# Performance work log

Measured on AMD Instinct MI355X. Metric: run time of the kernel, lower is better.

## Reference

```python
import jax, jax.numpy as jnp
import numpy as np
from math import factorial, sqrt

L_MAX = 3
L_MAX_OUT = 3
NUM_SHELLS = 3
NUM_SH = (L_MAX + 1) ** 2  # 16 spherical-harmonic kernel components
SPLIT = [2 * l + 1 for l in range(L_MAX + 1)]  # [1,3,5,7]


def _su2_cg(j1, m1, j2, m2, j3, m3):
    """Clebsch-Gordan coefficient <j1 m1 j2 m2 | j3 m3> via the Racah formula."""
    if m3 != m1 + m2:
        return 0.0
    f = factorial
    vmin = max(-j1 + j2 + m3, -j1 + m1, 0)
    vmax = min(j2 + j3 + m1, j3 - j1 + j2, j3 + m3)
    c = sqrt((2 * j3 + 1) * f(j3 + j1 - j2) * f(j3 - j1 + j2) * f(j1 + j2 - j3) / f(j1 + j2 + j3 + 1)
             * f(j3 + m3) * f(j3 - m3) / (f(j1 - m1) * f(j1 + m1) * f(j2 - m2) * f(j2 + m2)))
    s = 0.0
    for v in range(vmin, vmax + 1):
        s += (-1.0) ** (v + j2 + m2) * f(j2 + j3 + m1 - v) * f(j1 - m1 + v) / (
            f(v) * f(j3 - j1 + j2 - v) * f(j3 + m3 - v) * f(v + j1 - j2 - m3))
    return c * s


def _real_to_complex(l):
    q = np.zeros((2 * l + 1, 2 * l + 1), dtype=np.complex128)
    for m in range(-l, 0):
        q[l + m, l + abs(m)] = 1 / sqrt(2)
        q[l + m, l - abs(m)] = -1j / sqrt(2)
    q[l, l] = 1.0
    for m in range(1, l + 1):
        q[l + m, l + abs(m)] = (-1) ** m / sqrt(2)
        q[l + m, l - abs(m)] = 1j * (-1) ** m / sqrt(2)
    return (-1j) ** l * q  # phase makes the real-basis CG purely real


def _real_cg(j, l, J):
    # CG coupling tensor in the real spherical-harmonic basis, shape (2j+1, 2l+1, 2J+1)
    C = np.zeros((2 * j + 1, 2 * l + 1, 2 * J + 1))
    for m1 in range(-j, j + 1):
        for m2 in range(-l, l + 1):
            for m3 in range(-J, J + 1):
                C[j + m1, l + m2, J + m3] = _su2_cg(j, m1, l, m2, J, m3)
    Cr = np.einsum('ij,kl,mn,ikm->jln', _real_to_complex(j), _real_to_complex(l),
                   np.conj(_real_to_complex(J)), C.astype(np.complex128))
    return np.real(Cr).astype(np.float32)  # imaginary part vanishes by phase choice


_CG = {(j, l, J): jnp.asarray(_real_cg(j, l, J))
       for j in range(1, L_MAX + 1) for l in range(1, L_MAX + 1)
       for J in range(abs(j - l), min(j + l, L_MAX_OUT) + 1)}


def setup_inputs() -> dict:
    key = jax.random.key(0)
    ks = jax.random.split(key, 6)
    b, n_src, n_tgt, p, C = 2, 4096, 2048, 32, 32
    return {
        'f0': jax.random.normal(ks[0], (b, n_src, 1, C), jnp.float32),
        'f1': jax.random.normal(ks[1], (b, n_src, 3, C), jnp.float32),
        'f2': jax.random.normal(ks[2], (b, n_src, 5, C), jnp.float32),
        'f3': jax.random.normal(ks[3], (b, n_src, 7, C), jnp.float32),
        'kernels': jax.random.normal(ks[4], (b, n_tgt, p, NUM_SH, NUM_SHELLS), jnp.float32),
        'patches_idx': jax.random.randint(ks[5], (b, n_tgt, p), 0, n_src, jnp.int32),
    }


def reference(f0, f1, f2, f3, kernels, patches_idx):
    feats = [f0, f1, f2, f3]
    b, n_src = f0.shape[0], f0.shape[1]
    ch_split = [(2 * l + 1) * feats[l].shape[-1] for l in range(L_MAX + 1)]
    # flatten each degree block and concatenate: (b, n_src, sum (2l+1)*C_l)
    signal = jnp.concatenate([f.reshape(b, n_src, -1) for f in feats], axis=-1)
    # gather per-target-point patches: (b, n_tgt, p, Ct)
    patches = jax.vmap(lambda s, i: s[i])(signal, patches_idx)
    n_tgt, p = patches_idx.shape[1], patches_idx.shape[2]
    S = kernels.shape[-1]
    K = kernels.reshape(b, n_tgt, p, -1)  # (b, n_tgt, p, NUM_SH*S)
    # kernel-weighted patch contraction
    y = jnp.einsum('bvpy,bvpc->bvyc', K, patches)  # (b, n_tgt, NUM_SH*S, Ct)
    y_parts = jnp.split(y, list(np.cumsum(ch_split)[:-1]), axis=-1)
    sh_cuts = list(np.cumsum(SPLIT)[:-1])
    out = {J: [] for J in range(L_MAX_OUT + 1)}
    cg_terms = []
    for l in range(L_MAX + 1):
        Cl = feats[l].shape[-1]
        yi = y_parts[l].reshape(b, n_tgt, NUM_SH, S, 2 * l + 1, Cl)
        yi = jnp.transpose(yi, (0, 1, 2, 4, 3, 5)).reshape(b, n_tgt, NUM_SH, 2 * l + 1, S * Cl)
        yjs = jnp.split(yi, sh_cuts, axis=2)
        for j in range(L_MAX + 1):
            yij = yjs[j]  # (b, n_tgt, 2j+1, 2l+1, S*Cl)
            if l == 0:
                out[j].append(yij[:, :, :, 0, :])
            elif j == 0:
                out[l].append(yij[:, :, 0, :, :])
            else:
                cg_terms.append((j, l, yij))
    # sparse Clebsch-Gordan tensor-product decomposition
    for j, l, yij in cg_terms:
        for J in range(abs(j - l), min(j + l, L_MAX_OUT) + 1):
            out[J].append(jnp.einsum('xyz,bvxyc->bvzc', _CG[(j, l, J)], yij))
    return tuple(jnp.concatenate(out[J], axis=-1) for J in range(L_MAX_OUT + 1))
```

## Files before the change

### kernel.cpp

```cpp
#include <hip/hip_runtime.h>
#include <hip/hip_bf16.h>
#include <hip/hip_fp16.h>

#define NTGT 2048
#define NSRC 4096
#define NPATCH 32
#define NY 48
#define PITCH 136
#define NCG2 3524
#define NSLOTS 1280
#define DESC_OFF 16384

using short8 = __attribute__((ext_vector_type(8))) short;
using f32x4  = __attribute__((ext_vector_type(4))) float;

#define NTERMS 34
__constant__ int T_j[NTERMS]    = {0,1,2,3, 1,0,1,2,1,2,3,2,3, 2,0,1,2,3,1,2,3,1,2,3, 3,0,2,3,1,2,3,1,2,3};
__constant__ int T_l[NTERMS]    = {0,1,2,3, 0,1,1,1,2,2,2,3,3, 0,2,1,1,1,2,2,2,3,3,3, 0,3,1,1,2,2,2,3,3,3};
__constant__ int T_Jv[NTERMS]   = {0,0,0,0, 1,1,1,1,1,1,1,1,1, 2,2,2,2,2,2,2,2,2,2,2, 3,3,3,3,3,3,3,3,3,3};
__constant__ int T_col[NTERMS]  = {0,1,2,3, 0,1,2,3,4,5,6,7,8, 0,1,2,3,4,5,6,7,8,9,10, 0,1,2,3,4,5,6,7,8,9};
__constant__ int OUT_BASE[4] = {0, 1572864, 12189696, 33816576};
__constant__ int OUT_W[4]    = {384, 864, 1056, 960};
__constant__ int NJW_C[4]    = {384, 2592, 5280, 6720};
__constant__ int LI_L[16]  = {0,1,1,1,2,2,2,2,2,3,3,3,3,3,3,3};
__constant__ int LI_ML[16] = {0,0,1,2,0,1,2,3,4,0,1,2,3,4,5,6};
__constant__ int LI_WQ[16] = {1,3,3,3,5,5,5,5,5,7,7,7,7,7,7,7};
__constant__ int TERM_SLOT[NTERMS] = {1088,1024,384,0, 1094,1184,1030,896,768,390,256,128,6,
                                      1112,1202,1048,914,640,786,408,274,512,146,24,
                                      1142,1232,944,670,816,438,304,542,176,54};
__constant__ int CG2OFF4[NTERMS] = {0,0,3,10, 0,0,23,32,44,56,77,104,131,
                                    0,0,170,185,205,235,255,290,335,365,410,
                                    0,0,475,503,545,573,622,685,727,790};
__constant__ int RND_CLASS[20] = {0,0,1,1,2,2,3,3,4,4,5,5,6,6,7,7,8,9,9,9};
__constant__ signed char WAVE_RNDS[8][3] = {
  {0,17,-1},{1,16,-1},{2,8,-1},{3,9,18},{4,10,19},{5,11,-1},{6,14,13},{7,15,12}};

__device__ double factd(int n) { double r = 1.0; for (int i = 2; i <= n; ++i) r *= i; return r; }

__device__ double su2_cg(int j1, int m1, int j2, int m2, int j3, int m3) {
  if (m3 != m1 + m2) return 0.0;
  int vmin = max(max(-j1 + j2 + m3, -j1 + m1), 0);
  int vmax = min(min(j2 + j3 + m1, j3 - j1 + j2), j3 + m3);
  double cc = sqrt((2.0*j3 + 1.0) * factd(j3 + j1 - j2) * factd(j3 - j1 + j2) * factd(j1 + j2 - j3)
                   / factd(j1 + j2 + j3 + 1)
                   * factd(j3 + m3) * factd(j3 - m3)
                   / (factd(j1 - m1) * factd(j1 + m1) * factd(j2 - m2) * factd(j2 + m2)));
  double s = 0.0;
  for (int v = vmin; v <= vmax; ++v) {
    double sgn = ((v + j2 + m2) & 1) ? -1.0 : 1.0;
    s += sgn * factd(j2 + j3 + m1 - v) * factd(j1 - m1 + v)
         / (factd(v) * factd(j3 - j1 + j2 - v) * factd(j3 + m3 - v) * factd(v + j1 - j2 - m3));
  }
  return cc * s;
}

struct C2 { double re, im; };

__device__ C2 qent(int l, int r, int c) {
  double re = 0.0, im = 0.0;
  const double is2 = 0.70710678118654752440;
  int m = r - l;
  if (m < 0) {
    if (c == l - m) re = is2;
    else if (c == l + m) im = -is2;
  } else if (m == 0) {
    if (c == l) re = 1.0;
  } else {
    double sgn = (m & 1) ? -1.0 : 1.0;
    if (c == l + m) re = sgn * is2;
    else if (c == l - m) im = sgn * is2;
  }
  const double pr[4] = {1.0, 0.0, -1.0, 0.0};
  const double pi[4] = {0.0, -1.0, 0.0, 1.0};
  double a = pr[l & 3], bb = pi[l & 3];
  C2 o; o.re = re * a - im * bb; o.im = re * bb + im * a; return o;
}

__global__ void cg_init_kernel(__half* __restrict__ cg2) {
  __shared__ double su2_tab[49];
  const int t = blockIdx.x;
  const int j = T_j[t], l = T_l[t], J = T_Jv[t];
  if (j == 0 || l == 0) return;
  const int nj = 2*j + 1, nl = 2*l + 1, nJ = 2*J + 1;
  const int njnl = nj * nl, stride4 = (njnl + 3) >> 2;
  for (int ik = threadIdx.x; ik < njnl; ik += blockDim.x) {
    int i = ik / nl, k = ik - (ik / nl) * nl;
    int m = (i - j) + (k - l) + J;
    su2_tab[ik] = (m >= 0 && m <= 2*J) ? su2_cg(j, i - j, l, k - l, J, m - J) : 0.0;
  }
  __syncthreads();
  const int n = nJ * njnl;
  for (int e = threadIdx.x; e < n; e += blockDim.x) {
    const int z = e / njnl, rr = e - (e / njnl) * njnl;
    const int mj = rr / nl, ml = rr - (rr / nl) * nl;
    double acc = 0.0;
    for (int i = 0; i < nj; ++i) {
      for (int k = 0; k < nl; ++k) {
        int m = (i - j) + (k - l) + J;
        if (m < 0 || m > 2*J) continue;
        double s2 = su2_tab[i * nl + k];
        if (s2 == 0.0) continue;
        C2 qa = qent(j, i, mj), qb = qent(l, k, ml), qc = qent(J, m, z);
        double r1 = qa.re * qb.re - qa.im * qb.im;
        double i1 = qa.re * qb.im + qa.im * qb.re;
        acc += (r1 * qc.re + i1 * qc.im) * s2;
      }
    }
    cg2[(CG2OFF4[t] + z * stride4) * 4 + rr] = __float2half((float)acc);
  }
}

__global__ void desc_init_kernel(uint2* __restrict__ desc) {
  const int t = blockIdx.x;
  const int j = T_j[t], l = T_l[t], J = T_Jv[t];
  const int n = (2*J + 1) * 6;
  const int slot0 = TERM_SLOT[t];
  const bool cp = (j == 0 || l == 0);
  const int nl = 2*l + 1, njnl = (2*j + 1) * nl;
  const int stride4 = (njnl + 3) >> 2;
  for (int i = threadIdx.x; i < n; i += blockDim.x) {
    const int z = i / 6, r = i - (i / 6) * 6;
    const int s = r >> 1, ch4 = r & 1;
    const unsigned ob = (unsigned)(OUT_BASE[J] + T_col[t] * 96 + s * 32 + ch4 * 4 + z * OUT_W[J]);
    int ybase;
    if (!cp)         ybase = (j*j*3 + s) * PITCH + l*l*8 + ch4*4;
    else if (l == 0) ybase = ((j*j + z)*3 + s) * PITCH + ch4*4;
    else             ybase = s * PITCH + (l*l + z)*8 + ch4*4;
    const unsigned cgb4 = (unsigned)(CG2OFF4[t] + z * stride4);
    desc[slot0 + i] = make_uint2(ob,
        (unsigned)(ybase >> 2) | (cgb4 << 11) | ((unsigned)J << 21) | 0x80000000u);
  }
}

__device__ __forceinline__ unsigned bfb(float x) {
  union { __hip_bfloat16 h; unsigned short u; } c;
  c.h = __float2bfloat16(x);
  return (unsigned)c.u;
}

template<int JT, int LT>
__device__ __forceinline__ float4 pairc(const float4* __restrict__ yb4,
                                        const __half* __restrict__ cgp) {
  constexpr int nl = 2*LT + 1, njnl = (2*JT + 1) * nl;
  float a0 = 0.f, a1 = 0.f, a2 = 0.f, a3 = 0.f;
  #pragma unroll
  for (int e = 0; e < njnl; ++e) {
    const int mj = e / nl, ml = e - (e / nl) * nl;
    const float4 yq = yb4[mj * 102 + ml * 2];
    const float c = __half2float(cgp[e]);
    a0 = fmaf(c, yq.x, a0); a1 = fmaf(c, yq.y, a1);
    a2 = fmaf(c, yq.z, a2); a3 = fmaf(c, yq.w, a3);
  }
  float4 o; o.x = a0; o.y = a1; o.z = a2; o.w = a3; return o;
}

__global__ __launch_bounds__(512, 8) void sh_conv_kernel(
    const float* __restrict__ f0, const float* __restrict__ f1,
    const float* __restrict__ f2, const float* __restrict__ f3,
    const float* __restrict__ kern, const int* __restrict__ pidx,
    const __half* __restrict__ cg2, const uint2* __restrict__ desc,
    float* __restrict__ out) {
  __shared__ float y_lds[NY * PITCH];
  __shared__ __half cg_lds[NCG2];
  const int tid = threadIdx.x;
  const int lane = tid & 63, wid = tid >> 6;
  const int g = lane >> 4, lr = lane & 15;
  const int xcd  = blockIdx.x & 7;
  const int slot = blockIdx.x >> 3;
  const int bv   = ((slot >> 2) << 3) | xcd;
  const int cb   = slot & 3;
  const int b    = bv >> 11;

  const int* ip = pidx + (size_t)bv * NPATCH;
  int idx8[8];
  #pragma unroll
  for (int r = 0; r < 8; ++r) idx8[r] = ip[g * 8 + r];

  const float* kB = kern + (size_t)bv * (NPATCH * NY);
  float afv[3][8];
  #pragma unroll
  for (int m = 0; m < 3; ++m)
    #pragma unroll
    for (int r = 0; r < 8; ++r)
      afv[m][r] = kB[(g*8 + r) * NY + m*16 + lr];

  const int li  = wid * 2 + (lr >> 3);
  const int chl = lr & 7;
  const int l_  = LI_L[li], mlv = LI_ML[li], wq = LI_WQ[li];
  const float* fp = (l_ == 0) ? f0 : (l_ == 1) ? f1 : (l_ == 2) ? f2 : f3;
  const float* base = fp + ((size_t)b * NSRC) * (wq * 32) + mlv * 32 + cb * 8 + chl;
  float bv8[8];
  #pragma unroll
  for (int r = 0; r < 8; ++r) bv8[r] = base[(size_t)(idx8[r] * wq) << 5];

  {
    const unsigned* cgu = (const unsigned*)cg2;
    unsigned* cglu = (unsigned*)cg_lds;
    for (int i = tid; i < NCG2 / 2; i += 512) cglu[i] = cgu[i];
  }

  short8 afr[3];
  #pragma unroll
  for (int m = 0; m < 3; ++m) {
    short8 af;
    #pragma unroll
    for (int r = 0; r < 8; ++r) af[r] = (short)bfb(afv[m][r]);
    afr[m] = af;
  }
  short8 bfr;
  #pragma unroll
  for (int r = 0; r < 8; ++r) bfr[r] = (short)bfb(bv8[r]);

  f32x4 acc0 = {0.f,0.f,0.f,0.f}, acc1 = {0.f,0.f,0.f,0.f}, acc2 = {0.f,0.f,0.f,0.f};
  acc0 = __builtin_amdgcn_mfma_f32_16x16x32_bf16(afr[0], bfr, acc0, 0, 0, 0);
  acc1 = __builtin_amdgcn_mfma_f32_16x16x32_bf16(afr[1], bfr, acc1, 0, 0, 0);
  acc2 = __builtin_amdgcn_mfma_f32_16x16x32_bf16(afr[2], bfr, acc2, 0, 0, 0);

  #pragma unroll
  for (int q = 0; q < 4; ++q) {
    y_lds[(0*16 + g*4 + q) * PITCH + wid*16 + lr] = acc0[q];
    y_lds[(1*16 + g*4 + q) * PITCH + wid*16 + lr] = acc1[q];
    y_lds[(2*16 + g*4 + q) * PITCH + wid*16 + lr] = acc2[q];
  }

  __syncthreads();

  const int widu = __builtin_amdgcn_readfirstlane(wid);
  const float4* yall = (const float4*)y_lds;
  #pragma unroll 1
  for (int ri = 0; ri < 3; ++ri) {
    const int rnd = WAVE_RNDS[widu][ri];
    if (rnd < 0) break;
    const uint2 d = desc[(rnd << 6) | lane];
    const unsigned w1 = d.y;
    const float4* yb4 = yall + (w1 & 0x7FF);
    const __half* cgp = cg_lds + (((w1 >> 11) & 0x3FF) << 2);
    const int J = (w1 >> 21) & 3;
    float4 o;
    switch (RND_CLASS[rnd]) {
      case 0: o = pairc<3,3>(yb4, cgp); break;
      case 1: o = pairc<2,3>(yb4, cgp); break;
      case 2: o = pairc<3,2>(yb4, cgp); break;
      case 3: o = pairc<2,2>(yb4, cgp); break;
      case 4: o = pairc<1,3>(yb4, cgp); break;
      case 5: o = pairc<3,1>(yb4, cgp); break;
      case 6: o = pairc<1,2>(yb4, cgp); break;
      case 7: o = pairc<2,1>(yb4, cgp); break;
      case 8: o = pairc<1,1>(yb4, cgp); break;
      default: o = yb4[0]; break;
    }
    if (w1 >> 31)
      *(float4*)&out[(size_t)d.x + (size_t)bv * NJW_C[J] + cb * 8] = o;
  }
}

extern "C" void kernel_launch(void* const* d_in, const int* in_sizes, int n_in,
                              void* d_out, int out_size, void* d_ws, size_t ws_size,
                              hipStream_t stream) {
  const float* f0   = (const float*)d_in[0];
  const float* f1   = (const float*)d_in[1];
  const float* f2   = (const float*)d_in[2];
  const float* f3   = (const float*)d_in[3];
  const float* kern = (const float*)d_in[4];
  const int*   pidx = (const int*)d_in[5];
  float* out  = (float*)d_out;
  __half* cg2 = (__half*)d_ws;
  uint2* desc = (uint2*)((char*)d_ws + DESC_OFF);

  hipMemsetAsync(desc, 0, NSLOTS * sizeof(uint2), stream);
  hipLaunchKernelGGL(cg_init_kernel, dim3(NTERMS), dim3(256), 0, stream, cg2);
  hipLaunchKernelGGL(desc_init_kernel, dim3(NTERMS), dim3(64), 0, stream, desc);
  hipLaunchKernelGGL(sh_conv_kernel, dim3(4 * 2 * NTGT), dim3(512), 0, stream,
                     f0, f1, f2, f3, kern, pidx, cg2, desc, out);
}
```

Baseline: 197.5 us.

## Process two target points per block and prefetch second point's loads during first

Each block now handles two target voxels (bvA and bvB) instead of one, halving the grid. The kernel and feature gathers for the second voxel are issued before the first voxel's CG contraction phase, so their global-memory latency overlaps with that compute. The CG table copy into LDS is amortized over two voxels. The trade-offs are higher register pressure (launch bounds occupancy hint lowered from 8 to 6) and less parallelism per launch.

```diff
diff --git a/kernel.cpp b/kernel.cpp
--- a/kernel.cpp
+++ b/kernel.cpp
@@ -154,78 +154,11 @@
   float4 o; o.x = a0; o.y = a1; o.z = a2; o.w = a3; return o;
 }
 
-__global__ __launch_bounds__(512, 8) void sh_conv_kernel(
-    const float* __restrict__ f0, const float* __restrict__ f1,
-    const float* __restrict__ f2, const float* __restrict__ f3,
-    const float* __restrict__ kern, const int* __restrict__ pidx,
-    const __half* __restrict__ cg2, const uint2* __restrict__ desc,
-    float* __restrict__ out) {
-  __shared__ float y_lds[NY * PITCH];
-  __shared__ __half cg_lds[NCG2];
-  const int tid = threadIdx.x;
-  const int lane = tid & 63, wid = tid >> 6;
-  const int g = lane >> 4, lr = lane & 15;
-  const int xcd  = blockIdx.x & 7;
-  const int slot = blockIdx.x >> 3;
-  const int bv   = ((slot >> 2) << 3) | xcd;
-  const int cb   = slot & 3;
-  const int b    = bv >> 11;
-
-  const int* ip = pidx + (size_t)bv * NPATCH;
-  int idx8[8];
-  #pragma unroll
-  for (int r = 0; r < 8; ++r) idx8[r] = ip[g * 8 + r];
-
-  const float* kB = kern + (size_t)bv * (NPATCH * NY);
-  float afv[3][8];
-  #pragma unroll
-  for (int m = 0; m < 3; ++m)
-    #pragma unroll
-    for (int r = 0; r < 8; ++r)
-      afv[m][r] = kB[(g*8 + r) * NY + m*16 + lr];
-
-  const int li  = wid * 2 + (lr >> 3);
-  const int chl = lr & 7;
-  const int l_  = LI_L[li], mlv = LI_ML[li], wq = LI_WQ[li];
-  const float* fp = (l_ == 0) ? f0 : (l_ == 1) ? f1 : (l_ == 2) ? f2 : f3;
-  const float* base = fp + ((size_t)b * NSRC) * (wq * 32) + mlv * 32 + cb * 8 + chl;
-  float bv8[8];
-  #pragma unroll
-  for (int r = 0; r < 8; ++r) bv8[r] = base[(size_t)(idx8[r] * wq) << 5];
-
-  {
-    const unsigned* cgu = (const unsigned*)cg2;
-    unsigned* cglu = (unsigned*)cg_lds;
-    for (int i = tid; i < NCG2 / 2; i += 512) cglu[i] = cgu[i];
-  }
-
-  short8 afr[3];
-  #pragma unroll
-  for (int m = 0; m < 3; ++m) {
-    short8 af;
-    #pragma unroll
-    for (int r = 0; r < 8; ++r) af[r] = (short)bfb(afv[m][r]);
-    afr[m] = af;
-  }
-  short8 bfr;
-  #pragma unroll
-  for (int r = 0; r < 8; ++r) bfr[r] = (short)bfb(bv8[r]);
-
-  f32x4 acc0 = {0.f,0.f,0.f,0.f}, acc1 = {0.f,0.f,0.f,0.f}, acc2 = {0.f,0.f,0.f,0.f};
-  acc0 = __builtin_amdgcn_mfma_f32_16x16x32_bf16(afr[0], bfr, acc0, 0, 0, 0);
-  acc1 = __builtin_amdgcn_mfma_f32_16x16x32_bf16(afr[1], bfr, acc1, 0, 0, 0);
-  acc2 = __builtin_amdgcn_mfma_f32_16x16x32_bf16(afr[2], bfr, acc2, 0, 0, 0);
-
-  #pragma unroll
-  for (int q = 0; q < 4; ++q) {
-    y_lds[(0*16 + g*4 + q) * PITCH + wid*16 + lr] = acc0[q];
-    y_lds[(1*16 + g*4 + q) * PITCH + wid*16 + lr] = acc1[q];
-    y_lds[(2*16 + g*4 + q) * PITCH + wid*16 + lr] = acc2[q];
-  }
-
-  __syncthreads();
-
-  const int widu = __builtin_amdgcn_readfirstlane(wid);
+__device__ __forceinline__ void phase2(const float* __restrict__ y_lds,
+                                       const __half* __restrict__ cg_lds,
+                                       const uint2* __restrict__ desc,
+                                       float* __restrict__ out,
+                                       int widu, int lane, int bv, int cb) {
   const float4* yall = (const float4*)y_lds;
   #pragma unroll 1
   for (int ri = 0; ri < 3; ++ri) {
@@ -254,6 +187,131 @@
   }
 }
 
+__global__ __launch_bounds__(512, 6) void sh_conv_kernel(
+    const float* __restrict__ f0, const float* __restrict__ f1,
+    const float* __restrict__ f2, const float* __restrict__ f3,
+    const float* __restrict__ kern, const int* __restrict__ pidx,
+    const __half* __restrict__ cg2, const uint2* __restrict__ desc,
+    float* __restrict__ out) {
+  __shared__ float y_lds[NY * PITCH];
+  __shared__ __half cg_lds[NCG2];
+  const int tid = threadIdx.x;
+  const int lane = tid & 63, wid = tid >> 6;
+  const int g = lane >> 4, lr = lane & 15;
+  const int xcd = blockIdx.x & 7;
+  const int q   = blockIdx.x >> 3;
+  const int cb  = q & 3;
+  const int p   = q >> 2;
+  const int bvA = (p << 4) | xcd;
+  const int bvB = bvA | 8;
+  const int bA  = bvA >> 11, bB = bvB >> 11;
+
+  const int* ipA = pidx + (size_t)bvA * NPATCH;
+  const int* ipB = pidx + (size_t)bvB * NPATCH;
+  int idxA[8], idxB[8];
+  #pragma unroll
+  for (int r = 0; r < 8; ++r) idxA[r] = ipA[g * 8 + r];
+  #pragma unroll
+  for (int r = 0; r < 8; ++r) idxB[r] = ipB[g * 8 + r];
+
+  const float* kBa = kern + (size_t)bvA * (NPATCH * NY);
+  float afvA[3][8];
+  #pragma unroll
+  for (int m = 0; m < 3; ++m)
+    #pragma unroll
+    for (int r = 0; r < 8; ++r)
+      afvA[m][r] = kBa[(g*8 + r) * NY + m*16 + lr];
+
+  const int li  = wid * 2 + (lr >> 3);
+  const int chl = lr & 7;
+  const int l_  = LI_L[li], mlv = LI_ML[li], wq = LI_WQ[li];
+  const float* fp = (l_ == 0) ? f0 : (l_ == 1) ? f1 : (l_ == 2) ? f2 : f3;
+  const int coloff = mlv * 32 + cb * 8 + chl;
+  const float* baseA = fp + ((size_t)bA * NSRC) * (wq * 32) + coloff;
+  float avA[8];
+  #pragma unroll
+  for (int r = 0; r < 8; ++r) avA[r] = baseA[(size_t)(idxA[r] * wq) << 5];
+
+  {
+    const unsigned* cgu = (const unsigned*)cg2;
+    unsigned* cglu = (unsigned*)cg_lds;
+    for (int i = tid; i < NCG2 / 2; i += 512) cglu[i] = cgu[i];
+  }
+
+  short8 afr[3];
+  #pragma unroll
+  for (int m = 0; m < 3; ++m) {
+    short8 af;
+    #pragma unroll
+    for (int r = 0; r < 8; ++r) af[r] = (short)bfb(afvA[m][r]);
+    afr[m] = af;
+  }
+  short8 bfrA;
+  #pragma unroll
+  for (int r = 0; r < 8; ++r) bfrA[r] = (short)bfb(avA[r]);
+
+  {
+    f32x4 a0 = {0.f,0.f,0.f,0.f}, a1 = {0.f,0.f,0.f,0.f}, a2 = {0.f,0.f,0.f,0.f};
+    a0 = __builtin_amdgcn_mfma_f32_16x16x32_bf16(afr[0], bfrA, a0, 0, 0, 0);
+    a1 = __builtin_amdgcn_mfma_f32_16x16x32_bf16(afr[1], bfrA, a1, 0, 0, 0);
+    a2 = __builtin_amdgcn_mfma_f32_16x16x32_bf16(afr[2], bfrA, a2, 0, 0, 0);
+    #pragma unroll
+    for (int qq = 0; qq < 4; ++qq) {
+      y_lds[(0*16 + g*4 + qq) * PITCH + wid*16 + lr] = a0[qq];
+      y_lds[(1*16 + g*4 + qq) * PITCH + wid*16 + lr] = a1[qq];
+      y_lds[(2*16 + g*4 + qq) * PITCH + wid*16 + lr] = a2[qq];
+    }
+  }
+
+  const float* kBb = kern + (size_t)bvB * (NPATCH * NY);
+  float afvB[3][8];
+  #pragma unroll
+  for (int m = 0; m < 3; ++m)
+    #pragma unroll
+    for (int r = 0; r < 8; ++r)
+      afvB[m][r] = kBb[(g*8 + r) * NY + m*16 + lr];
+  const float* baseB = fp + ((size_t)bB * NSRC) * (wq * 32) + coloff;
+  float avB[8];
+  #pragma unroll
+  for (int r = 0; r < 8; ++r) avB[r] = baseB[(size_t)(idxB[r] * wq) << 5];
+
+  asm volatile("s_waitcnt lgkmcnt(0)" ::: "memory");
+  __builtin_amdgcn_s_barrier();
+  __builtin_amdgcn_sched_barrier(0);
+
+  const int widu = __builtin_amdgcn_readfirstlane(wid);
+  phase2(y_lds, cg_lds, desc, out, widu, lane, bvA, cb);
+
+  __syncthreads();
+
+  #pragma unroll
+  for (int m = 0; m < 3; ++m) {
+    short8 af;
+    #pragma unroll
+    for (int r = 0; r < 8; ++r) af[r] = (short)bfb(afvB[m][r]);
+    afr[m] = af;
+  }
+  short8 bfrB;
+  #pragma unroll
+  for (int r = 0; r < 8; ++r) bfrB[r] = (short)bfb(avB[r]);
+  {
+    f32x4 a0 = {0.f,0.f,0.f,0.f}, a1 = {0.f,0.f,0.f,0.f}, a2 = {0.f,0.f,0.f,0.f};
+    a0 = __builtin_amdgcn_mfma_f32_16x16x32_bf16(afr[0], bfrB, a0, 0, 0, 0);
+    a1 = __builtin_amdgcn_mfma_f32_16x16x32_bf16(afr[1], bfrB, a1, 0, 0, 0);
+    a2 = __builtin_amdgcn_mfma_f32_16x16x32_bf16(afr[2], bfrB, a2, 0, 0, 0);
+    #pragma unroll
+    for (int qq = 0; qq < 4; ++qq) {
+      y_lds[(0*16 + g*4 + qq) * PITCH + wid*16 + lr] = a0[qq];
+      y_lds[(1*16 + g*4 + qq) * PITCH + wid*16 + lr] = a1[qq];
+      y_lds[(2*16 + g*4 + qq) * PITCH + wid*16 + lr] = a2[qq];
+    }
+  }
+
+  __syncthreads();
+
+  phase2(y_lds, cg_lds, desc, out, widu, lane, bvB, cb);
+}
+
 extern "C" void kernel_launch(void* const* d_in, const int* in_sizes, int n_in,
                               void* d_out, int out_size, void* d_ws, size_t ws_size,
                               hipStream_t stream) {
@@ -270,6 +328,6 @@
   hipMemsetAsync(desc, 0, NSLOTS * sizeof(uint2), stream);
   hipLaunchKernelGGL(cg_init_kernel, dim3(NTERMS), dim3(256), 0, stream, cg2);
   hipLaunchKernelGGL(desc_init_kernel, dim3(NTERMS), dim3(64), 0, stream, desc);
-  hipLaunchKernelGGL(sh_conv_kernel, dim3(4 * 2 * NTGT), dim3(512), 0, stream,
+  hipLaunchKernelGGL(sh_conv_kernel, dim3(4 * NTGT), dim3(512), 0, stream,
                      f0, f1, f2, f3, kern, pidx, cg2, desc, out);
 }
```

After: 374.1 us. +89.5%, slower.

## Pair adjacent output components per lane to reuse Y loads across two CG rows

Applied to the files above, without the earlier changes.

Each lane now computes two output m-components (z pairs) of the same CG term, sharing each Y float4 LDS load between two CG coefficient streams. The descriptor layout changes to pair slots, the number of rounds drops from twenty to eleven, and waves run at most two rounds. Occupancy in launch bounds drops from 8 to 6 waves per SIMD to make room for the doubled accumulators. The goal is to halve LDS reads of Y and the number of descriptor rounds, at the cost of more registers and possibly uneven wave load.

```diff
diff --git a/kernel.cpp b/kernel.cpp
--- a/kernel.cpp
+++ b/kernel.cpp
@@ -8,7 +8,8 @@
 #define NY 48
 #define PITCH 136
 #define NCG2 3524
-#define NSLOTS 1280
+#define NROUNDS 11
+#define NSLOTS (NROUNDS*128)
 #define DESC_OFF 16384
 
 using short8 = __attribute__((ext_vector_type(8))) short;
@@ -25,15 +26,14 @@
 __constant__ int LI_L[16]  = {0,1,1,1,2,2,2,2,2,3,3,3,3,3,3,3};
 __constant__ int LI_ML[16] = {0,0,1,2,0,1,2,3,4,0,1,2,3,4,5,6};
 __constant__ int LI_WQ[16] = {1,3,3,3,5,5,5,5,5,7,7,7,7,7,7,7};
-__constant__ int TERM_SLOT[NTERMS] = {1088,1024,384,0, 1094,1184,1030,896,768,390,256,128,6,
-                                      1112,1202,1048,914,640,786,408,274,512,146,24,
-                                      1142,1232,944,670,816,438,304,542,176,54};
 __constant__ int CG2OFF4[NTERMS] = {0,0,3,10, 0,0,23,32,44,56,77,104,131,
                                     0,0,170,185,205,235,255,290,335,365,410,
                                     0,0,475,503,545,573,622,685,727,790};
-__constant__ int RND_CLASS[20] = {0,0,1,1,2,2,3,3,4,4,5,5,6,6,7,7,8,9,9,9};
-__constant__ signed char WAVE_RNDS[8][3] = {
-  {0,17,-1},{1,16,-1},{2,8,-1},{3,9,18},{4,10,19},{5,11,-1},{6,14,13},{7,15,12}};
+__constant__ int T_rnd[NTERMS]   = {9,8,3,0, 9,10,8,7,6,3,2,1,0, 9,10,8,7,5,6,3,2,4,1,0, 9,10,7,5,6,3,2,4,1,0};
+__constant__ int T_sbase[NTERMS] = {0,0,0,0, 6,0,12,0,0,12,0,0,12, 24,18,36,24,0,24,36,24,0,24,36, 54,48,60,36,60,72,60,36,60,72};
+__constant__ int RND_CLASS[NROUNDS] = {0,1,2,3,4,5,6,7,8,9,9};
+__constant__ signed char WAVE_RNDS[8][2] = {
+  {0,-1},{1,-1},{2,-1},{3,8},{4,6},{5,7},{9,-1},{10,-1}};
 
 __device__ double factd(int n) { double r = 1.0; for (int i = 2; i <= n; ++i) r *= i; return r; }
 
@@ -113,11 +113,13 @@
 __global__ void desc_init_kernel(uint2* __restrict__ desc) {
   const int t = blockIdx.x;
   const int j = T_j[t], l = T_l[t], J = T_Jv[t];
-  const int n = (2*J + 1) * 6;
-  const int slot0 = TERM_SLOT[t];
+  const int NJ = 2*J + 1;
+  const int n = NJ * 6;
   const bool cp = (j == 0 || l == 0);
   const int nl = 2*l + 1, njnl = (2*j + 1) * nl;
   const int stride4 = (njnl + 3) >> 2;
+  const int np = (NJ + 1) >> 1;
+  const int rnd = T_rnd[t], sb = T_sbase[t];
   for (int i = threadIdx.x; i < n; i += blockDim.x) {
     const int z = i / 6, r = i - (i / 6) * 6;
     const int s = r >> 1, ch4 = r & 1;
@@ -127,7 +129,10 @@
     else if (l == 0) ybase = ((j*j + z)*3 + s) * PITCH + ch4*4;
     else             ybase = s * PITCH + (l*l + z)*8 + ch4*4;
     const unsigned cgb4 = (unsigned)(CG2OFF4[t] + z * stride4);
-    desc[slot0 + i] = make_uint2(ob,
+    int slot;
+    if (cp) slot = sb + i;
+    else    slot = sb + r * 2 * np + ((z >> 1) << 1) + (z & 1);
+    desc[(rnd << 7) + slot] = make_uint2(ob,
         (unsigned)(ybase >> 2) | (cgb4 << 11) | ((unsigned)J << 21) | 0x80000000u);
   }
 }
@@ -139,22 +144,29 @@
 }
 
 template<int JT, int LT>
-__device__ __forceinline__ float4 pairc(const float4* __restrict__ yb4,
-                                        const __half* __restrict__ cgp) {
+__device__ __forceinline__ void pairc2(const float4* __restrict__ yb4,
+                                       const __half* __restrict__ cgA,
+                                       const __half* __restrict__ cgB,
+                                       float4& o0, float4& o1) {
   constexpr int nl = 2*LT + 1, njnl = (2*JT + 1) * nl;
   float a0 = 0.f, a1 = 0.f, a2 = 0.f, a3 = 0.f;
+  float b0 = 0.f, b1 = 0.f, b2 = 0.f, b3 = 0.f;
   #pragma unroll
   for (int e = 0; e < njnl; ++e) {
     const int mj = e / nl, ml = e - (e / nl) * nl;
     const float4 yq = yb4[mj * 102 + ml * 2];
-    const float c = __half2float(cgp[e]);
-    a0 = fmaf(c, yq.x, a0); a1 = fmaf(c, yq.y, a1);
-    a2 = fmaf(c, yq.z, a2); a3 = fmaf(c, yq.w, a3);
-  }
-  float4 o; o.x = a0; o.y = a1; o.z = a2; o.w = a3; return o;
-}
-
-__global__ __launch_bounds__(512, 8) void sh_conv_kernel(
+    const float cA = __half2float(cgA[e]);
+    const float cB = __half2float(cgB[e]);
+    a0 = fmaf(cA, yq.x, a0); a1 = fmaf(cA, yq.y, a1);
+    a2 = fmaf(cA, yq.z, a2); a3 = fmaf(cA, yq.w, a3);
+    b0 = fmaf(cB, yq.x, b0); b1 = fmaf(cB, yq.y, b1);
+    b2 = fmaf(cB, yq.z, b2); b3 = fmaf(cB, yq.w, b3);
+  }
+  o0.x = a0; o0.y = a1; o0.z = a2; o0.w = a3;
+  o1.x = b0; o1.y = b1; o1.z = b2; o1.w = b3;
+}
+
+__global__ __launch_bounds__(512, 6) void sh_conv_kernel(
     const float* __restrict__ f0, const float* __restrict__ f1,
     const float* __restrict__ f2, const float* __restrict__ f3,
     const float* __restrict__ kern, const int* __restrict__ pidx,
@@ -228,29 +240,34 @@
   const int widu = __builtin_amdgcn_readfirstlane(wid);
   const float4* yall = (const float4*)y_lds;
   #pragma unroll 1
-  for (int ri = 0; ri < 3; ++ri) {
+  for (int ri = 0; ri < 2; ++ri) {
     const int rnd = WAVE_RNDS[widu][ri];
     if (rnd < 0) break;
-    const uint2 d = desc[(rnd << 6) | lane];
-    const unsigned w1 = d.y;
-    const float4* yb4 = yall + (w1 & 0x7FF);
-    const __half* cgp = cg_lds + (((w1 >> 11) & 0x3FF) << 2);
-    const int J = (w1 >> 21) & 3;
-    float4 o;
+    const uint4 dd = *(const uint4*)(desc + (rnd << 7) + (lane << 1));
+    const unsigned wa = dd.y, wb = dd.w;
+    const float4* yb4 = yall + (wa & 0x7FF);
+    const __half* cgA = cg_lds + (((wa >> 11) & 0x3FF) << 2);
+    const __half* cgB = cg_lds + (((wb >> 11) & 0x3FF) << 2);
+    float4 o0, o1;
     switch (RND_CLASS[rnd]) {
-      case 0: o = pairc<3,3>(yb4, cgp); break;
-      case 1: o = pairc<2,3>(yb4, cgp); break;
-      case 2: o = pairc<3,2>(yb4, cgp); break;
-      case 3: o = pairc<2,2>(yb4, cgp); break;
-      case 4: o = pairc<1,3>(yb4, cgp); break;
-      case 5: o = pairc<3,1>(yb4, cgp); break;
-      case 6: o = pairc<1,2>(yb4, cgp); break;
-      case 7: o = pairc<2,1>(yb4, cgp); break;
-      case 8: o = pairc<1,1>(yb4, cgp); break;
-      default: o = yb4[0]; break;
+      case 0: pairc2<3,3>(yb4, cgA, cgB, o0, o1); break;
+      case 1: pairc2<2,3>(yb4, cgA, cgB, o0, o1); break;
+      case 2: pairc2<3,2>(yb4, cgA, cgB, o0, o1); break;
+      case 3: pairc2<2,2>(yb4, cgA, cgB, o0, o1); break;
+      case 4: pairc2<1,3>(yb4, cgA, cgB, o0, o1); break;
+      case 5: pairc2<3,1>(yb4, cgA, cgB, o0, o1); break;
+      case 6: pairc2<1,2>(yb4, cgA, cgB, o0, o1); break;
+      case 7: pairc2<2,1>(yb4, cgA, cgB, o0, o1); break;
+      case 8: pairc2<1,1>(yb4, cgA, cgB, o0, o1); break;
+      default:
+        o0 = yall[wa & 0x7FF];
+        o1 = yall[wb & 0x7FF];
+        break;
     }
-    if (w1 >> 31)
-      *(float4*)&out[(size_t)d.x + (size_t)bv * NJW_C[J] + cb * 8] = o;
+    if (wa >> 31)
+      *(float4*)&out[(size_t)dd.x + (size_t)bv * NJW_C[(wa >> 21) & 3] + cb * 8] = o0;
+    if (wb >> 31)
+      *(float4*)&out[(size_t)dd.z + (size_t)bv * NJW_C[(wb >> 21) & 3] + cb * 8] = o1;
   }
 }
 
```

After: 198.5 us. Within noise of the previous version (+0.5%).
